# Optimization experiments

Hardware: AMD Instinct MI355X
Metric: run time of the kernel (lower is better)

Reference implementation:

```python
import jax, jax.numpy as jnp
import numpy as np

B, L, D_MODEL, N_HEADS = 8, 256, 2048, 8
D_HEAD = D_MODEL // N_HEADS  # 256 == L, required by DeltaRuleOperator broadcasting
ALPHA0, BETA0 = 0.1, 0.9      # delta_rule_strength, 1 - strength
LN_EPS = 1e-5


def setup_inputs() -> dict:
    k = jax.random.key(0)
    ks = jax.random.split(k, 8)
    s = 0.02
    return {
        "query": jax.random.normal(ks[0], (B, L, D_MODEL), jnp.float32),
        "key": jax.random.normal(ks[1], (B, L, D_MODEL), jnp.float32),
        "value": jax.random.normal(ks[2], (B, L, D_MODEL), jnp.float32),
        "Wq": jax.random.normal(ks[3], (D_MODEL, D_MODEL), jnp.float32) * s,
        "Wk": jax.random.normal(ks[4], (D_MODEL, D_MODEL), jnp.float32) * s,
        "Wv": jax.random.normal(ks[5], (D_MODEL, D_MODEL), jnp.float32) * s,
        "Wo": jax.random.normal(ks[6], (D_MODEL, D_MODEL), jnp.float32) * s,
        "bo": jnp.zeros((D_MODEL,), jnp.float32),
        "ln_g": jnp.ones((D_MODEL,), jnp.float32),
        "ln_b": jnp.zeros((D_MODEL,), jnp.float32),
        "alpha": jnp.asarray(ALPHA0, jnp.float32),
        "beta": jnp.asarray(BETA0, jnp.float32),
    }


def reference(query, key, value, Wq, Wk, Wv, Wo, bo, ln_g, ln_b, alpha, beta):
    Bs, Ls, D = query.shape
    H, Dh = N_HEADS, D // N_HEADS

    def proj(x, W):  # torch Linear: x @ W.T, split heads -> [B,H,L,Dh]
        return (x @ W.T).reshape(Bs, Ls, H, Dh).transpose(0, 2, 1, 3)

    Q = proj(query, Wq)
    K = proj(key, Wk)
    V = proj(value, Wv)

    # DeltaRuleOperator, applied sequentially per head (buffer mutates across heads)
    kv = jnp.einsum('bhld,bhmd->bhlm', K, V)  # [B,H,L,L] with L == Dh
    kv_heads = jnp.moveaxis(kv, 1, 0)          # [H,B,L,L]

    def cs_step(cs, kv_h):
        # cumulative_state = beta*cs + alpha*detach(mean(kv)); head uses pre-update cs
        new = beta * cs + alpha * jax.lax.stop_gradient(kv_h.mean(axis=(0, 1)))
        return new, cs

    _, cs_seq = jax.lax.scan(cs_step, jnp.zeros((Dh,), query.dtype), kv_heads)  # [H,Dh]
    cs_b = cs_seq[None, :, None, :]                       # [1,H,1,Dh]
    q_mod = Q * (cs_b + alpha * (kv - cs_b))              # delta-rule modulated queries

    # elu feature map
    phi = lambda x: jax.nn.elu(x) + 1.0
    pq, pk = phi(q_mod), phi(K)

    def time_major(x):  # [B,H,L,Dh] -> [L, B*H, Dh]
        return x.reshape(Bs * H, Ls, Dh).transpose(1, 0, 2)

    pq_t, pk_t, v_t = time_major(pq), time_major(pk), time_major(V)

    def step(carry, xs):
        S, Z = carry                        # S:[N,Dh,Dh], Z:[N,Dh]
        q_i, k_i, v_i = xs                  # each [N,Dh]
        S = S + k_i[:, :, None] * v_i[:, None, :]
        Z = Z + k_i
        num = jnp.einsum('nf,nfd->nd', q_i, S)
        den = jnp.maximum(jnp.sum(q_i * Z, axis=-1), 1e-8)
        return (S, Z), num / den[:, None]

    N = Bs * H
    S0 = jnp.zeros((N, Dh, Dh), query.dtype)
    Z0 = jnp.zeros((N, Dh), query.dtype)
    _, outs = jax.lax.scan(step, (S0, Z0), (pq_t, pk_t, v_t))  # [L,N,Dh]

    attn = outs.transpose(1, 0, 2).reshape(Bs, H, Ls, Dh)
    attn = attn.transpose(0, 2, 1, 3).reshape(Bs, Ls, D)       # concat heads

    o = attn @ Wo.T + bo                  # out_proj (dropout is identity in eval)
    x = query + o                          # residual + LayerNorm
    mu = x.mean(-1, keepdims=True)
    var = jnp.mean((x - mu) ** 2, axis=-1, keepdims=True)
    return (x - mu) / jnp.sqrt(var + LN_EPS) * ln_g + ln_b
```

## Files before the change

### kernel.cpp

```cpp
#include <hip/hip_runtime.h>
#include <hip/hip_bf16.h>

using u16 = unsigned short;

typedef __bf16 bf16x8 __attribute__((ext_vector_type(8)));
typedef float  f32x4  __attribute__((ext_vector_type(4)));

__device__ __forceinline__ float b2f(u16 u) {
  union { unsigned u; float f; } v; v.u = ((unsigned)u) << 16; return v.f;
}
__device__ __forceinline__ u16 f2b(float f) {
  union { float f; unsigned u; } v; v.f = f;
  unsigned r = v.u + 0x7fffu + ((v.u >> 16) & 1u);
  return (u16)(r >> 16);
}

__device__ __forceinline__ void gld_lds16(const void* g, void* l) {
  __builtin_amdgcn_global_load_lds(
      (__attribute__((address_space(1))) void*)(unsigned long long)(g),
      (__attribute__((address_space(3))) void*)(unsigned long long)(l),
      16, 0, 0);
}

template <int EPI, int BK>
__global__ __launch_bounds__(256) void gemm_bt(
    const u16* __restrict__ A, int lda, long sA1, long sA2,
    const u16* __restrict__ B, int ldb, long sB1, long sB2,
    void* __restrict__ Cv, int ldc, long sC1, long sC2,
    int K, int HDIV,
    const float* __restrict__ bias, const float* __restrict__ resid,
    float* __restrict__ partOut) {
  __shared__ __align__(16) u16 lds[2 * 128 * BK];
  __shared__ float denS[128];
  const int t = threadIdx.x;
  const int lane = t & 63;
  const int wave = t >> 6;
  const int wm = wave >> 1, wn = wave & 1;
  const int laneM = lane & 15, quad = lane >> 4;
  const int zb = blockIdx.z / HDIV, zh = blockIdx.z % HDIV;

  int bx = blockIdx.x, by = blockIdx.y;
  if (EPI == 2) { by = (bx >= 1) ? 1 : 0; bx = (bx == 2) ? 1 : 0; }
  const int kEnd = (EPI == 3) ? ((by + 1) * 128 < K ? (by + 1) * 128 : K) : K;

  const u16* Abase = A + zb * sA1 + zh * sA2 + (long)by * 128 * lda;
  const u16* Bbase = B + zb * sB1 + zh * sB2 + (long)bx * 128 * ldb;

  constexpr int STEPS = BK / 16;
  constexpr int RPS = 2048 / BK;
  constexpr int KK = BK / 32;
  const int sRow = (BK == 64) ? (t >> 3) : (t >> 2);
  const int sg = (BK == 64) ? (t & 7) : (t & 3);
  const int swz = (BK == 64) ? (sg ^ (sRow & 7)) : (sg ^ ((sRow >> 1) & 3));
  const int sc = swz * 8;

  f32x4 acc[4][4];
#pragma unroll
  for (int i = 0; i < 4; ++i)
#pragma unroll
    for (int j = 0; j < 4; ++j) acc[i][j] = (f32x4){0.f, 0.f, 0.f, 0.f};
  float dsum[4] = {0.f, 0.f, 0.f, 0.f};

  for (int k0 = 0; k0 < kEnd; k0 += BK) {
#pragma unroll
    for (int p = 0; p < STEPS; ++p)
      gld_lds16(Abase + (long)(p * RPS + sRow) * lda + k0 + sc,
                &lds[p * 2048 + t * 8]);
#pragma unroll
    for (int p = 0; p < STEPS; ++p)
      gld_lds16(Bbase + (long)(p * RPS + sRow) * ldb + k0 + sc,
                &lds[128 * BK + p * 2048 + t * 8]);
    __syncthreads();
    bf16x8 af[KK][4], bfv[KK][4];
#pragma unroll
    for (int kk = 0; kk < KK; ++kk) {
      int perm8;
      if (BK == 64) perm8 = ((kk * 4 + quad) ^ (laneM & 7)) * 8;
      else          perm8 = (quad ^ ((laneM >> 1) & 3)) * 8;
#pragma unroll
      for (int i = 0; i < 4; ++i) {
        af[kk][i] = *(const bf16x8*)&lds[(wm * 64 + i * 16 + laneM) * BK + perm8];
        bfv[kk][i] =
            *(const bf16x8*)&lds[128 * BK + (wn * 64 + i * 16 + laneM) * BK + perm8];
      }
    }
    if (EPI == 3) {
#pragma unroll
      for (int kk = 0; kk < KK; ++kk)
#pragma unroll
        for (int i = 0; i < 4; ++i) {
          union { bf16x8 v; u16 s[8]; } u; u.v = af[kk][i];
          float ds = 0.f;
#pragma unroll
          for (int e = 0; e < 8; ++e) ds += b2f(u.s[e]);
          dsum[i] += ds;
        }
    }
#pragma unroll
    for (int kk = 0; kk < KK; ++kk)
#pragma unroll
      for (int i = 0; i < 4; ++i)
#pragma unroll
        for (int j = 0; j < 4; ++j)
          acc[i][j] = __builtin_amdgcn_mfma_f32_16x16x32_bf16(
              af[kk][i], bfv[kk][j], acc[i][j], 0, 0, 0);
    __syncthreads();
  }

  if (EPI == 3) {
#pragma unroll
    for (int i = 0; i < 4; ++i) {
      float s = dsum[i];
      s += __shfl_xor(s, 16);
      s += __shfl_xor(s, 32);
      if (wn == 0 && quad == 0)
        denS[wm * 64 + i * 16 + laneM] = fmaxf(s, 1e-8f);
    }
    __syncthreads();
  }

  if (EPI == 1) {
#pragma unroll
    for (int j = 0; j < 4; ++j) {
      float s = 0.f;
#pragma unroll
      for (int i = 0; i < 4; ++i)
#pragma unroll
        for (int r = 0; r < 4; ++r) s += acc[i][j][r];
      s += __shfl_xor(s, 16);
      s += __shfl_xor(s, 32);
      if (quad == 0)
        atomicAdd(&partOut[zh * 256 + bx * 128 + wn * 64 + j * 16 + laneM], s);
    }
  }

  const long cOff = zb * sC1 + zh * sC2;
  const int colB = bx * 128 + wn * 64;
#pragma unroll
  for (int i = 0; i < 4; ++i) {
#pragma unroll
    for (int j = 0; j < 4; ++j) {
#pragma unroll
      for (int r = 0; r < 4; ++r) {
        const int lrow = wm * 64 + i * 16 + quad * 4 + r;
        const int row = by * 128 + lrow;
        const int col = colB + j * 16 + laneM;
        const long idx = cOff + (long)row * ldc + col;
        float v = acc[i][j][r];
        if (EPI == 0 || EPI == 1) {
          ((u16*)Cv)[idx] = f2b(v);
        } else if (EPI == 2) {
          ((u16*)Cv)[idx] = f2b(col <= row ? v : 0.0f);
        } else if (EPI == 3) {
          ((u16*)Cv)[idx] = f2b(v / denS[lrow]);
        } else {
          ((float*)Cv)[idx] =
              (zb == 0) ? v + bias[col] + resid[(long)row * ldc + col] : v;
        }
      }
    }
  }
}

__global__ __launch_bounds__(256) void convert7(
    const float* __restrict__ s0, const float* __restrict__ s1,
    const float* __restrict__ s2, const float* __restrict__ s3,
    const float* __restrict__ s4, const float* __restrict__ s5,
    const float* __restrict__ s6, u16* __restrict__ dst) {
  long idx = (long)blockIdx.x * 256 + threadIdx.x;
  int seg = (int)(idx >> 20);
  long off = (idx & 1048575) << 2;
  const float* s;
  switch (seg) {
    case 0: s = s0; break; case 1: s = s1; break; case 2: s = s2; break;
    case 3: s = s3; break; case 4: s = s4; break; case 5: s = s5; break;
    default: s = s6;
  }
  float4 v = *(const float4*)(s + off);
  ushort4 o;
  o.x = f2b(v.x); o.y = f2b(v.y); o.z = f2b(v.z); o.w = f2b(v.w);
  *(ushort4*)(dst + (long)seg * 4194304 + off) = o;
}

__global__ __launch_bounds__(256) void cs_kernel(
    const float* __restrict__ part, float* __restrict__ cs,
    const float* __restrict__ alphaP, const float* __restrict__ betaP) {
  int m = threadIdx.x;
  float alpha = *alphaP, beta = *betaP;
  float c = 0.f;
  for (int h = 0; h < 8; ++h) {
    cs[h * 256 + m] = c;
    c = beta * c + alpha * (part[h * 256 + m] * (1.0f / 2048.0f));
  }
}

__global__ __launch_bounds__(256) void pqpk_kernel(
    const u16* __restrict__ Qp, const u16* __restrict__ Kp,
    const u16* __restrict__ kv, const float* __restrict__ cs,
    const float* __restrict__ alphaP, u16* __restrict__ pq,
    u16* __restrict__ pk) {
  long idx = (long)blockIdx.x * 256 + threadIdx.x;
  int d = idx & 255, l = (int)((idx >> 8) & 255), h = (int)((idx >> 16) & 7),
      b = (int)(idx >> 19);
  float alpha = *alphaP;
  long pidx = ((long)(b * 256 + l)) * 2048 + h * 256 + d;
  float Qv = b2f(Qp[pidx]);
  float kvv = b2f(kv[idx]);
  float csv = cs[h * 256 + d];
  float qm = Qv * (csv + alpha * (kvv - csv));
  pq[idx] = f2b(qm > 0.f ? qm + 1.f : expf(qm));
  float Kv = b2f(Kp[pidx]);
  pk[idx] = f2b(Kv > 0.f ? Kv + 1.f : expf(Kv));
}

__global__ __launch_bounds__(256) void vtrans_kernel(const u16* __restrict__ Vp,
                                                     u16* __restrict__ Vt) {
  __shared__ u16 tile[32][33];
  int z = blockIdx.z, b = z >> 3, h = z & 7;
  int jT = blockIdx.x * 32, dT = blockIdx.y * 32;
  int tx = threadIdx.x, ty = threadIdx.y;
#pragma unroll
  for (int ii = 0; ii < 4; ++ii) {
    int j = jT + ty + ii * 8, d = dT + tx;
    tile[ty + ii * 8][tx] = Vp[(long)(b * 256 + j) * 2048 + h * 256 + d];
  }
  __syncthreads();
#pragma unroll
  for (int ii = 0; ii < 4; ++ii) {
    int d = dT + ty + ii * 8, j = jT + tx;
    Vt[(long)z * 65536 + d * 256 + j] = tile[tx][ty + ii * 8];
  }
}

__global__ __launch_bounds__(256) void ln_kernel(
    const float* __restrict__ x0, const float* __restrict__ x1,
    const float* __restrict__ g, const float* __restrict__ bb,
    float* __restrict__ out) {
  int row = blockIdx.x, t = threadIdx.x;
  const float4* xr0 = (const float4*)(x0 + (long)row * 2048);
  const float4* xr1 = (const float4*)(x1 + (long)row * 2048);
  float4 a0 = xr0[t], b0 = xr1[t], a1 = xr0[t + 256], b1 = xr1[t + 256];
  float4 v0, v1;
  v0.x = a0.x + b0.x; v0.y = a0.y + b0.y; v0.z = a0.z + b0.z; v0.w = a0.w + b0.w;
  v1.x = a1.x + b1.x; v1.y = a1.y + b1.y; v1.z = a1.z + b1.z; v1.w = a1.w + b1.w;
  float s = v0.x + v0.y + v0.z + v0.w + v1.x + v1.y + v1.z + v1.w;
  float ss = v0.x * v0.x + v0.y * v0.y + v0.z * v0.z + v0.w * v0.w +
             v1.x * v1.x + v1.y * v1.y + v1.z * v1.z + v1.w * v1.w;
  for (int o = 32; o; o >>= 1) { s += __shfl_xor(s, o); ss += __shfl_xor(ss, o); }
  __shared__ float a1s[4], a2s[4];
  int wave = t >> 6, lane = t & 63;
  if (lane == 0) { a1s[wave] = s; a2s[wave] = ss; }
  __syncthreads();
  s = a1s[0] + a1s[1] + a1s[2] + a1s[3];
  ss = a2s[0] + a2s[1] + a2s[2] + a2s[3];
  float mu = s * (1.f / 2048.f);
  float var = ss * (1.f / 2048.f) - mu * mu;
  float rstd = rsqrtf(var + 1e-5f);
  const float4* g4 = (const float4*)g;
  const float4* b4 = (const float4*)bb;
  float4* orow = (float4*)(out + (long)row * 2048);
  float4 gg = g4[t], bv = b4[t], r;
  r.x = (v0.x - mu) * rstd * gg.x + bv.x;
  r.y = (v0.y - mu) * rstd * gg.y + bv.y;
  r.z = (v0.z - mu) * rstd * gg.z + bv.z;
  r.w = (v0.w - mu) * rstd * gg.w + bv.w;
  orow[t] = r;
  gg = g4[t + 256]; bv = b4[t + 256];
  r.x = (v1.x - mu) * rstd * gg.x + bv.x;
  r.y = (v1.y - mu) * rstd * gg.y + bv.y;
  r.z = (v1.z - mu) * rstd * gg.z + bv.z;
  r.w = (v1.w - mu) * rstd * gg.w + bv.w;
  orow[t + 256] = r;
}

extern "C" void kernel_launch(void* const* d_in, const int* in_sizes, int n_in,
                              void* d_out, int out_size, void* d_ws,
                              size_t ws_size, hipStream_t stream) {
  const float* query = (const float*)d_in[0];
  const float* key = (const float*)d_in[1];
  const float* value = (const float*)d_in[2];
  const float* Wq = (const float*)d_in[3];
  const float* Wk = (const float*)d_in[4];
  const float* Wv = (const float*)d_in[5];
  const float* Wo = (const float*)d_in[6];
  const float* bo = (const float*)d_in[7];
  const float* ln_g = (const float*)d_in[8];
  const float* ln_b = (const float*)d_in[9];
  const float* alphaP = (const float*)d_in[10];
  const float* betaP = (const float*)d_in[11];

  char* ws = (char*)d_ws;
  const long SZ = 8388608;
  u16* qb = (u16*)(ws);
  u16* Wb = (u16*)(ws + 3 * SZ);
  u16* Qp = (u16*)(ws + 7 * SZ);
  u16* kvb = (u16*)(ws + 10 * SZ);
  u16* pq = (u16*)(ws + 12 * SZ);
  u16* pk = (u16*)(ws + 13 * SZ);
  u16* Vt = (u16*)(ws + 14 * SZ);
  u16* attnb = (u16*)(ws + 15 * SZ);
  u16* Ab = (u16*)(ws + 10 * SZ);
  float* x0 = (float*)(ws + 12 * SZ);
  float* x1 = (float*)(ws);
  float* part = (float*)(ws + 16 * SZ);
  float* cs = (float*)(ws + 16 * SZ + 16384);

  u16* Kp = Qp + 4194304;
  u16* Vp = Qp + 8388608;
  u16* Wob = Wb + 3 * 4194304;

  hipMemsetAsync(part, 0, 8 * 256 * sizeof(float), stream);

  convert7<<<28672, 256, 0, stream>>>(query, key, value, Wq, Wk, Wv, Wo, qb);

  gemm_bt<0, 32><<<dim3(16, 16, 3), 256, 0, stream>>>(
      qb, 2048, 4194304L, 0L, Wb, 2048, 4194304L, 0L, (void*)Qp, 2048,
      4194304L, 0L, 2048, 1, nullptr, nullptr, nullptr);

  gemm_bt<1, 64><<<dim3(2, 2, 64), 256, 0, stream>>>(
      Kp, 2048, 524288L, 256L, Vp, 2048, 524288L, 256L, (void*)kvb, 256,
      524288L, 65536L, 256, 8, nullptr, nullptr, part);

  cs_kernel<<<1, 256, 0, stream>>>(part, cs, alphaP, betaP);

  pqpk_kernel<<<16384, 256, 0, stream>>>(Qp, Kp, kvb, cs, alphaP, pq, pk);

  gemm_bt<2, 64><<<dim3(3, 1, 64), 256, 0, stream>>>(
      pq, 256, 524288L, 65536L, pk, 256, 524288L, 65536L, (void*)Ab, 256,
      524288L, 65536L, 256, 8, nullptr, nullptr, nullptr);

  vtrans_kernel<<<dim3(8, 8, 64), dim3(32, 8), 0, stream>>>(Vp, Vt);

  gemm_bt<3, 64><<<dim3(2, 2, 64), 256, 0, stream>>>(
      Ab, 256, 524288L, 65536L, Vt, 256, 524288L, 65536L, (void*)attnb, 2048,
      524288L, 256L, 256, 8, nullptr, nullptr, nullptr);

  gemm_bt<4, 32><<<dim3(16, 16, 2), 256, 0, stream>>>(
      attnb, 2048, 1024L, 0L, Wob, 2048, 1024L, 0L, (void*)x0, 2048,
      -25165824L, 0L, 1024, 1, bo, query, nullptr);

  ln_kernel<<<2048, 256, 0, stream>>>(x0, x1, ln_g, ln_b, (float*)d_out);
}
```

Before: 338.8 us.

## Add 256x256-tile triple-buffered GEMM for QKV and output projections

Adds a new 512-thread GEMM kernel with 256x256 output tiles, triple-buffered LDS fed by direct global-to-LDS loads, XOR-swizzled layout, and blockIdx remapping for L2 locality. It replaces the 128-tile gemm_bt for the QKV projection and the split-K output projection. Larger tiles raise arithmetic intensity and cut global traffic per FLOP. In exchange there are fewer blocks (192 and 128 on a large CU count), high register pressure from 128 accumulators per thread, and large LDS use.

Result: no change. 344.2 us (+1.6%).

```diff
diff --git a/kernel.cpp b/kernel.cpp
--- a/kernel.cpp
+++ b/kernel.cpp
@@ -156,6 +156,155 @@
         } else {
           ((float*)Cv)[idx] =
               (zb == 0) ? v + bias[col] + resid[(long)row * ldc + col] : v;
+        }
+      }
+    }
+  }
+}
+
+template <int EPI>
+__global__ __launch_bounds__(512) void gemm256(
+    const u16* __restrict__ A, int lda, long sA1,
+    const u16* __restrict__ B, int ldb, long sB1,
+    void* __restrict__ Cv, int ldc, long sC1, int K,
+    const float* __restrict__ bias, const float* __restrict__ resid) {
+  __shared__ __align__(16) u16 ldsA[3][8192];
+  __shared__ __align__(16) u16 ldsB[3][8192];
+  const int t = threadIdx.x;
+  const int lane = t & 63, wave = t >> 6;
+  const int wm = wave >> 2, wn = wave & 3;
+  const int laneM = lane & 15, quad = lane >> 4;
+
+  const int cpx = gridDim.x >> 3;
+  const int id2 = (blockIdx.x & 7) * cpx + (blockIdx.x >> 3);
+  const int bx = id2 & 7, by = (id2 >> 3) & 7, z = id2 >> 6;
+
+  const u16* Ag = A + (long)z * sA1 + (long)by * 256 * lda;
+  const u16* Bg = B + (long)z * sB1 + (long)bx * 256 * ldb;
+
+  const int nt = K >> 5;
+  const int rg = (quad ^ ((laneM >> 1) & 3)) * 8;
+  const int rowA = wm * 128 + laneM;
+  const int rowB = wn * 64 + laneM;
+
+  f32x4 acc[8][4];
+#pragma unroll
+  for (int i = 0; i < 8; ++i)
+#pragma unroll
+    for (int j = 0; j < 4; ++j) acc[i][j] = (f32x4){0.f, 0.f, 0.f, 0.f};
+
+  {
+#pragma unroll
+    for (int p = 0; p < 2; ++p) {
+      const int chunk = p * 512 + t, row = chunk >> 2;
+      const int c = (chunk & 3) ^ ((row >> 1) & 3);
+      gld_lds16(Ag + row * lda + c * 8, &ldsA[0][chunk * 8]);
+    }
+#pragma unroll
+    for (int p = 0; p < 2; ++p) {
+      const int chunk = p * 512 + t, row = chunk >> 2;
+      const int c = (chunk & 3) ^ ((row >> 1) & 3);
+      gld_lds16(Bg + row * ldb + c * 8, &ldsB[0][chunk * 8]);
+    }
+#pragma unroll
+    for (int p = 0; p < 2; ++p) {
+      const int chunk = p * 512 + t, row = chunk >> 2;
+      const int c = (chunk & 3) ^ ((row >> 1) & 3);
+      gld_lds16(Ag + row * lda + 32 + c * 8, &ldsA[1][chunk * 8]);
+    }
+#pragma unroll
+    for (int p = 0; p < 2; ++p) {
+      const int chunk = p * 512 + t, row = chunk >> 2;
+      const int c = (chunk & 3) ^ ((row >> 1) & 3);
+      gld_lds16(Bg + row * ldb + 32 + c * 8, &ldsB[1][chunk * 8]);
+    }
+  }
+  asm volatile("s_waitcnt vmcnt(4)" ::: "memory");
+  __builtin_amdgcn_s_barrier();
+
+  int buf = 0, sbuf = 2;
+  for (int tau = 0; tau < nt; ++tau) {
+    const u16* la = &ldsA[buf][0];
+    const u16* lb = &ldsB[buf][0];
+    const bool st = (tau + 2) < nt;
+    const int ks = (tau + 2) << 5;
+    bf16x8 af[4], bv[4];
+
+#pragma unroll
+    for (int m = 0; m < 4; ++m)
+      af[m] = *(const bf16x8*)&la[(rowA + m * 16) * 32 + rg];
+#pragma unroll
+    for (int n = 0; n < 4; ++n)
+      bv[n] = *(const bf16x8*)&lb[(rowB + n * 16) * 32 + rg];
+    if (st) {
+#pragma unroll
+      for (int p = 0; p < 2; ++p) {
+        const int chunk = p * 512 + t, row = chunk >> 2;
+        const int c = (chunk & 3) ^ ((row >> 1) & 3);
+        gld_lds16(Ag + row * lda + ks + c * 8, &ldsA[sbuf][chunk * 8]);
+      }
+    }
+    __builtin_amdgcn_s_barrier();
+    asm volatile("s_waitcnt lgkmcnt(0)" ::: "memory");
+    __builtin_amdgcn_s_setprio(1);
+#pragma unroll
+    for (int m = 0; m < 4; ++m)
+#pragma unroll
+      for (int n = 0; n < 4; ++n)
+        acc[m][n] = __builtin_amdgcn_mfma_f32_16x16x32_bf16(af[m], bv[n],
+                                                            acc[m][n], 0, 0, 0);
+    __builtin_amdgcn_s_setprio(0);
+    __builtin_amdgcn_s_barrier();
+
+#pragma unroll
+    for (int m = 0; m < 4; ++m)
+      af[m] = *(const bf16x8*)&la[(rowA + 64 + m * 16) * 32 + rg];
+    if (st) {
+#pragma unroll
+      for (int p = 0; p < 2; ++p) {
+        const int chunk = p * 512 + t, row = chunk >> 2;
+        const int c = (chunk & 3) ^ ((row >> 1) & 3);
+        gld_lds16(Bg + row * ldb + ks + c * 8, &ldsB[sbuf][chunk * 8]);
+      }
+    }
+    __builtin_amdgcn_s_barrier();
+    asm volatile("s_waitcnt lgkmcnt(0)" ::: "memory");
+    __builtin_amdgcn_s_setprio(1);
+#pragma unroll
+    for (int m = 0; m < 4; ++m)
+#pragma unroll
+      for (int n = 0; n < 4; ++n)
+        acc[4 + m][n] = __builtin_amdgcn_mfma_f32_16x16x32_bf16(
+            af[m], bv[n], acc[4 + m][n], 0, 0, 0);
+    __builtin_amdgcn_s_setprio(0);
+
+    if (tau < nt - 1) {
+      if (st) asm volatile("s_waitcnt vmcnt(4)" ::: "memory");
+      else    asm volatile("s_waitcnt vmcnt(0)" ::: "memory");
+      __builtin_amdgcn_s_barrier();
+    }
+    buf = (buf == 2) ? 0 : buf + 1;
+    sbuf = (sbuf == 2) ? 0 : sbuf + 1;
+  }
+
+  const long cOff = (long)z * sC1;
+  const int colB = bx * 256 + wn * 64;
+  const int rowBase = by * 256 + wm * 128;
+#pragma unroll
+  for (int i = 0; i < 8; ++i) {
+#pragma unroll
+    for (int j = 0; j < 4; ++j) {
+#pragma unroll
+      for (int r = 0; r < 4; ++r) {
+        const int row = rowBase + i * 16 + quad * 4 + r;
+        const int col = colB + j * 16 + laneM;
+        const long idx = cOff + (long)row * ldc + col;
+        float v = acc[i][j][r];
+        if (EPI == 0) {
+          ((u16*)Cv)[idx] = f2b(v);
+        } else {
+          ((float*)Cv)[idx] =
+              (z == 0) ? v + bias[col] + resid[(long)row * ldc + col] : v;
         }
       }
     }
@@ -313,9 +462,9 @@
 
   convert7<<<28672, 256, 0, stream>>>(query, key, value, Wq, Wk, Wv, Wo, qb);
 
-  gemm_bt<0, 32><<<dim3(16, 16, 3), 256, 0, stream>>>(
-      qb, 2048, 4194304L, 0L, Wb, 2048, 4194304L, 0L, (void*)Qp, 2048,
-      4194304L, 0L, 2048, 1, nullptr, nullptr, nullptr);
+  gemm256<0><<<dim3(192, 1, 1), 512, 0, stream>>>(
+      qb, 2048, 4194304L, Wb, 2048, 4194304L, (void*)Qp, 2048, 4194304L,
+      2048, nullptr, nullptr);
 
   gemm_bt<1, 64><<<dim3(2, 2, 64), 256, 0, stream>>>(
       Kp, 2048, 524288L, 256L, Vp, 2048, 524288L, 256L, (void*)kvb, 256,
@@ -335,9 +484,9 @@
       Ab, 256, 524288L, 65536L, Vt, 256, 524288L, 65536L, (void*)attnb, 2048,
       524288L, 256L, 256, 8, nullptr, nullptr, nullptr);
 
-  gemm_bt<4, 32><<<dim3(16, 16, 2), 256, 0, stream>>>(
-      attnb, 2048, 1024L, 0L, Wob, 2048, 1024L, 0L, (void*)x0, 2048,
-      -25165824L, 0L, 1024, 1, bo, query, nullptr);
+  gemm256<4><<<dim3(128, 1, 1), 512, 0, stream>>>(
+      attnb, 2048, 1024L, Wob, 2048, 1024L, (void*)x0, 2048, -25165824L,
+      1024, bo, query);
 
   ln_kernel<<<2048, 256, 0, stream>>>(x0, x1, ln_g, ln_b, (float*)d_out);
 }
```
